# Performance work log

Hardware: AMD Instinct MI355X
Metric: run time of the kernel (lower is better)

## Reference

```python
import jax, jax.numpy as jnp
import numpy as np

D_MODEL = 1024
N_HEADS = 16
HEAD_DIM = D_MODEL // N_HEADS
WINDOW = 128
N_PERSIST = 4
KSIZE = 3


def _make_mask(L):
    """[T,T] additive mask, T = N_PERSIST + L. Persistent rows: causal among
    persistent tokens. Sequence rows: all persistent cols + sliding causal window."""
    T = N_PERSIST + L
    r = jnp.arange(T)[:, None]
    c = jnp.arange(T)[None, :]
    seq_allowed = (c < N_PERSIST) | ((c >= jnp.maximum(N_PERSIST, r - WINDOW + 1)) & (c <= r))
    allowed = jnp.where(r < N_PERSIST, c <= r, seq_allowed)
    return jnp.where(allowed, 0.0, -jnp.inf).astype(jnp.float32)


def _causal_dw_conv(y, w, b):
    # y: [B,T,D] -> depthwise causal conv1d + SiLU -> [B,T,D]
    y = y.transpose(0, 2, 1)  # [B,D,T]
    y = jax.lax.conv_general_dilated(
        y, w, window_strides=(1,), padding=[(KSIZE - 1, 0)],
        feature_group_count=D_MODEL, dimension_numbers=('NCH', 'OIH', 'NCH'))
    y = jax.nn.silu(y + b[None, :, None])
    return y.transpose(0, 2, 1)


def _l2norm(y, eps=1e-12):
    n = jnp.linalg.norm(y, axis=-1, keepdims=True)
    return y / jnp.maximum(n, eps)


def setup_inputs() -> dict:
    key = jax.random.key(0)
    ks = jax.random.split(key, 12)
    s = 1.0 / np.sqrt(D_MODEL)
    return {
        'x': jax.random.normal(ks[0], (1, 2048, D_MODEL), jnp.float32),
        'persistent_memory': jax.random.normal(ks[1], (1, N_PERSIST, D_MODEL), jnp.float32) * 0.02,
        'Wq': jax.random.normal(ks[2], (D_MODEL, D_MODEL), jnp.float32) * s,
        'Wk': jax.random.normal(ks[3], (D_MODEL, D_MODEL), jnp.float32) * s,
        'Wv': jax.random.normal(ks[4], (D_MODEL, D_MODEL), jnp.float32) * s,
        'Wo': jax.random.normal(ks[5], (D_MODEL, D_MODEL), jnp.float32) * s,
        'q_conv_w': jax.random.normal(ks[6], (D_MODEL, 1, KSIZE), jnp.float32) * 0.3,
        'q_conv_b': jax.random.normal(ks[7], (D_MODEL,), jnp.float32) * 0.02,
        'k_conv_w': jax.random.normal(ks[8], (D_MODEL, 1, KSIZE), jnp.float32) * 0.3,
        'k_conv_b': jax.random.normal(ks[9], (D_MODEL,), jnp.float32) * 0.02,
        'v_conv_w': jax.random.normal(ks[10], (D_MODEL, 1, KSIZE), jnp.float32) * 0.3,
        'v_conv_b': jax.random.normal(ks[11], (D_MODEL,), jnp.float32) * 0.02,
    }


def reference(x, persistent_memory, Wq, Wk, Wv, Wo,
              q_conv_w, q_conv_b, k_conv_w, k_conv_b, v_conv_w, v_conv_b):
    B, L, D = x.shape
    T = L + N_PERSIST
    scale = HEAD_DIM ** -0.5
    xp = jnp.concatenate([jnp.broadcast_to(persistent_memory, (B, N_PERSIST, D)), x], axis=1)
    Q = xp @ Wq.T
    K = xp @ Wk.T
    V = xp @ Wv.T
    Q = _causal_dw_conv(Q, q_conv_w, q_conv_b)
    K = _causal_dw_conv(K, k_conv_w, k_conv_b)
    V = _causal_dw_conv(V, v_conv_w, v_conv_b)
    Q = _l2norm(Q)
    K = _l2norm(K)
    # [B,H,T,hd]
    Q = Q.reshape(B, T, N_HEADS, HEAD_DIM).transpose(0, 2, 1, 3)
    K = K.reshape(B, T, N_HEADS, HEAD_DIM).transpose(0, 2, 1, 3)
    V = V.reshape(B, T, N_HEADS, HEAD_DIM).transpose(0, 2, 1, 3)
    scores = jnp.einsum('bhqd,bhkd->bhqk', Q, K) * scale + _make_mask(L)[None, None]
    attn = jax.nn.softmax(scores, axis=-1)
    out = jnp.einsum('bhqk,bhkd->bhqd', attn, V)
    out = out.transpose(0, 2, 1, 3).reshape(B, T, D) @ Wo.T
    return out[:, N_PERSIST:, :]
```

## Files before the change

### kernel.cpp

```cpp
#include <hip/hip_runtime.h>
#include <math.h>

typedef unsigned short u16;
typedef unsigned int   u32;
typedef unsigned long long u64;
typedef __attribute__((ext_vector_type(8))) short bf16x8;
typedef __attribute__((ext_vector_type(4))) float f32x4;
typedef __attribute__((ext_vector_type(4))) int i32x4;

#define TTOT  2052
#define NPERS 4
#define LSEQ  2048
#define WIN   128
#define NHEAD 16
#define HDIM  64
#define DM    1024
#define MPAD  2176

__device__ __forceinline__ float bf2f(u16 u) {
    union { unsigned int i; float f; } v; v.i = ((unsigned int)u) << 16; return v.f;
}
__device__ __forceinline__ u16 f2bf(float f) {
    union { float f; unsigned int i; } v; v.f = f;
    unsigned int r = (v.i + 0x7fffu + ((v.i >> 16) & 1u)) >> 16;
    return (u16)r;
}
__device__ __forceinline__ u32 pk2(float lo, float hi) {
    return (u32)f2bf(lo) | ((u32)f2bf(hi) << 16);
}

__device__ __forceinline__ void glds16(const u16* g, u16* l) {
    __builtin_amdgcn_global_load_lds(
        (__attribute__((address_space(1))) void*)(g),
        (__attribute__((address_space(3))) void*)(l),
        16, 0, 0);
}

__global__ __launch_bounds__(256) void cvt(const float* __restrict__ x, const float* __restrict__ pm,
    const float* __restrict__ Wq, const float* __restrict__ Wk, const float* __restrict__ Wv,
    const float* __restrict__ Wo,
    u16* __restrict__ xp, u16* __restrict__ Wcat, u16* __restrict__ Woh)
{
    const int z = blockIdx.y;
    const int u = blockIdx.x * 256 + threadIdx.x;
    if (z == 0) {
        if (u >= TTOT * 256) return;
        const size_t e = (size_t)u * 4;
        const int row = (int)(e >> 10), c = (int)(e & 1023);
        const float* s = (row < NPERS) ? (pm + (size_t)row * DM + c)
                                       : (x + (size_t)(row - NPERS) * DM + c);
        f32x4 v = *(const f32x4*)s;
        *(u64*)(xp + e) = (u64)pk2(v[0], v[1]) | ((u64)pk2(v[2], v[3]) << 32);
    } else {
        if (u >= 256 * DM) return;
        const size_t e = (size_t)u * 4;
        const float* s; u16* d;
        if (z == 1)      { s = Wq + e; d = Wcat + e; }
        else if (z == 2) { s = Wk + e; d = Wcat + (size_t)DM * DM + e; }
        else if (z == 3) { s = Wv + e; d = Wcat + 2 * (size_t)DM * DM + e; }
        else             { s = Wo + e; d = Woh + e; }
        f32x4 v = *(const f32x4*)s;
        *(u64*)d = (u64)pk2(v[0], v[1]) | ((u64)pk2(v[2], v[3]) << 32);
    }
}

template<int TM, int TN, bool OF32>
__device__ __forceinline__ void gemm_lds(const u16* __restrict__ Ablk, const u16* __restrict__ Bblk,
                                         void* __restrict__ Cbase, int mlim)
{
    __shared__ __align__(16) u16 As[TM * 32];
    __shared__ __align__(16) u16 Bs[TN * 32];
    const int tid  = threadIdx.x;
    const int lane = tid & 63;
    const int l15  = lane & 15, quad = lane >> 4;
    constexpr int RM = TM / 32, RN = TN / 32;
    const int wm = (tid >> 7) * (TM / 2);
    const int wn = ((tid >> 6) & 1) * (TN / 2);
    const int wb = tid & 192;

    f32x4 acc[RM][RN];
    #pragma unroll
    for (int i = 0; i < RM; i++)
        #pragma unroll
        for (int j = 0; j < RN; j++) acc[i][j] = (f32x4){0.f, 0.f, 0.f, 0.f};

    constexpr int LA = (TM * 32) / 2048;
    constexpr int LB = (TN * 32) / 2048;

    for (int kk = 0; kk < DM; kk += 32) {
        #pragma unroll
        for (int i = 0; i < LA; i++) {
            const int e = i * 256 + tid;
            glds16(Ablk + (size_t)(e >> 2) * DM + kk + (e & 3) * 8,
                   As + (size_t)(i * 256 + wb) * 8);
        }
        #pragma unroll
        for (int i = 0; i < LB; i++) {
            const int e = i * 256 + tid;
            glds16(Bblk + (size_t)(e >> 2) * DM + kk + (e & 3) * 8,
                   Bs + (size_t)(i * 256 + wb) * 8);
        }
        __syncthreads();
        bf16x8 af[RM], bfr[RN];
        #pragma unroll
        for (int i = 0; i < RM; i++) af[i]  = *(const bf16x8*)&As[(wm + i * 16 + l15) * 32 + quad * 8];
        #pragma unroll
        for (int j = 0; j < RN; j++) bfr[j] = *(const bf16x8*)&Bs[(wn + j * 16 + l15) * 32 + quad * 8];
        #pragma unroll
        for (int i = 0; i < RM; i++)
            #pragma unroll
            for (int j = 0; j < RN; j++)
                acc[i][j] = __builtin_amdgcn_mfma_f32_16x16x32_bf16(af[i], bfr[j], acc[i][j], 0, 0, 0);
        __syncthreads();
    }

    #pragma unroll
    for (int i = 0; i < RM; i++) {
        const int m0 = wm + i * 16 + quad * 4;
        #pragma unroll
        for (int j = 0; j < RN; j++) {
            const int n = wn + j * 16 + l15;
            #pragma unroll
            for (int r = 0; r < 4; r++) {
                const int m = m0 + r;
                if (m < mlim) {
                    if (OF32) ((float*)Cbase)[(size_t)m * DM + n] = acc[i][j][r];
                    else      ((u16*)Cbase)[(size_t)m * DM + n]   = f2bf(acc[i][j][r]);
                }
            }
        }
    }
}

__global__ __launch_bounds__(256) void gemm_qkv(const u16* __restrict__ xp, const u16* __restrict__ Wcat,
    u16* __restrict__ Qr, u16* __restrict__ Kr, u16* __restrict__ Vr)
{
    const int Mb = blockIdx.x * 128;
    const int nb = blockIdx.y;
    u16* C = (nb < 8) ? Qr : (nb < 16) ? Kr : Vr;
    const int Ncol = (nb & 7) * 128;
    gemm_lds<128, 128, false>(xp + (size_t)Mb * DM,
                              Wcat + (size_t)nb * 128 * DM,
                              (void*)(C + (size_t)Mb * DM + Ncol),
                              TTOT - Mb);
}

__global__ __launch_bounds__(256) void gemm_out(const u16* __restrict__ AO, const u16* __restrict__ Woh,
                                                float* __restrict__ Cout)
{
    const int Mb = blockIdx.x * 64, Nb = blockIdx.y * 128;
    gemm_lds<64, 128, true>(AO + (size_t)Mb * DM, Woh + (size_t)Nb * DM,
                            (void*)(Cout + (size_t)Mb * DM + Nb), 64);
}

__global__ __launch_bounds__(256) void conv_silu_norm(
    const u16* __restrict__ Qr, const u16* __restrict__ Kr, const u16* __restrict__ Vr,
    const float* __restrict__ qw, const float* __restrict__ qb,
    const float* __restrict__ kw, const float* __restrict__ kb,
    const float* __restrict__ vw, const float* __restrict__ vb,
    u16* __restrict__ Qc, u16* __restrict__ Kc, u16* __restrict__ Vc)
{
    const int t = blockIdx.x;
    const int z = blockIdx.y;
    const u16* raw; const float *w, *b; u16* out;
    if (z == 0)      { raw = Qr; w = qw; b = qb; out = Qc; }
    else if (z == 1) { raw = Kr; w = kw; b = kb; out = Kc; }
    else             { raw = Vr; w = vw; b = vb; out = Vc; }

    const int tid = threadIdx.x;
    const int d0  = tid * 4;

    const u16* r0 = raw + (size_t)t * DM + d0;
    u64 c0 = *(const u64*)r0;
    u64 c1 = (t >= 1) ? *(const u64*)(r0 - DM)     : 0ULL;
    u64 c2 = (t >= 2) ? *(const u64*)(r0 - 2 * DM) : 0ULL;
    const f32x4 bias = *(const f32x4*)(b + d0);
    const f32x4 w0v  = *(const f32x4*)(w + 3 * d0);
    const f32x4 w1v  = *(const f32x4*)(w + 3 * d0 + 4);
    const f32x4 w2v  = *(const f32x4*)(w + 3 * d0 + 8);
    const float warr[12] = {w0v[0], w0v[1], w0v[2], w0v[3],
                            w1v[0], w1v[1], w1v[2], w1v[3],
                            w2v[0], w2v[1], w2v[2], w2v[3]};

    float vals[4];
    float ss = 0.f;
    #pragma unroll
    for (int c = 0; c < 4; c++) {
        float acc = bias[c];
        acc += warr[3*c + 2] * bf2f((u16)(c0 >> (16 * c)));
        acc += warr[3*c + 1] * bf2f((u16)(c1 >> (16 * c)));
        acc += warr[3*c + 0] * bf2f((u16)(c2 >> (16 * c)));
        const float y = acc / (1.f + __expf(-acc));
        vals[c] = y;
        ss += y * y;
    }
    float inv = 1.f;
    if (z < 2) {
        #pragma unroll
        for (int off = 32; off > 0; off >>= 1) ss += __shfl_down(ss, off, 64);
        __shared__ float red[4];
        const int wv = tid >> 6, ln = tid & 63;
        if (ln == 0) red[wv] = ss;
        __syncthreads();
        const float tot = red[0] + red[1] + red[2] + red[3];
        inv = 1.f / fmaxf(sqrtf(tot), 1e-12f);
    }
    u64 o = 0;
    #pragma unroll
    for (int c = 0; c < 4; c++) o |= (u64)f2bf(vals[c] * inv) << (16 * c);
    *(u64*)(out + (size_t)t * DM + d0) = o;
}

#define QT     64
#define KTILES 13
#define KROWS  208
#define KPAD   224
#define KSTR   72
#define VSTR   232

__global__ __launch_bounds__(256) void attn(const u16* __restrict__ Q, const u16* __restrict__ K,
                                            const u16* __restrict__ V, u16* __restrict__ AO)
{
    const int h  = blockIdx.y;
    const int qb = blockIdx.x * QT;
    const int kstart = max(NPERS, qb + NPERS - (WIN - 1));
    const int nk = NPERS + (qb + NPERS + QT - 1) - kstart + 1;

    __shared__ __align__(16) u16 KP[KROWS * KSTR];
    __shared__ __align__(16) u16 Vt[64 * VSTR];
    u16* Ks = KP;
    u16* Ps = KP;

    const int tid = threadIdx.x;

    for (int c = tid; c < KROWS * 8; c += 256) {
        const int i = c >> 3, off = (c & 7) * 8;
        if (i < nk) {
            const int g = (i < NPERS) ? i : (kstart + i - NPERS);
            *(i32x4*)&Ks[i * KSTR + off] = *(const i32x4*)&K[(size_t)g * DM + h * HDIM + off];
        }
    }
    {
        const int d = tid & 63, w4 = tid >> 6;
        for (int i2 = w4 * 2; i2 < KPAD; i2 += 8) {
            u16 a = 0, b = 0;
            if (i2 < nk)     { const int g = (i2     < NPERS) ? i2     : (kstart + i2     - NPERS); a = V[(size_t)g * DM + h * HDIM + d]; }
            if (i2 + 1 < nk) { const int g = (i2 + 1 < NPERS) ? i2 + 1 : (kstart + i2 + 1 - NPERS); b = V[(size_t)g * DM + h * HDIM + d]; }
            *(u32*)&Vt[d * VSTR + i2] = (u32)a | ((u32)b << 16);
        }
    }
    __syncthreads();

    const int wv = tid >> 6, lane = tid & 63, l15 = lane & 15, quad = lane >> 4;
    const int qloc0 = wv * 16;

    const int tqrow = qb + qloc0 + l15 + NPERS;
    const bf16x8 qa0 = *(const bf16x8*)&Q[(size_t)tqrow * DM + h * HDIM + quad * 8];
    const bf16x8 qa1 = *(const bf16x8*)&Q[(size_t)tqrow * DM + h * HDIM + 32 + quad * 8];

    f32x4 st[KTILES];
    #pragma unroll
    for (int t = 0; t < KTILES; t++) {
        const bf16x8 kb0 = *(const bf16x8*)&Ks[(t * 16 + l15) * KSTR + quad * 8];
        const bf16x8 kb1 = *(const bf16x8*)&Ks[(t * 16 + l15) * KSTR + 32 + quad * 8];
        f32x4 z = (f32x4){0.f, 0.f, 0.f, 0.f};
        z = __builtin_amdgcn_mfma_f32_16x16x32_bf16(qa0, kb0, z, 0, 0, 0);
        z = __builtin_amdgcn_mfma_f32_16x16x32_bf16(qa1, kb1, z, 0, 0, 0);
        st[t] = z;
    }

    const float scale = 0.125f;
    float mrow[4] = {-INFINITY, -INFINITY, -INFINITY, -INFINITY};
    #pragma unroll
    for (int t = 0; t < KTILES; t++) {
        const int i  = t * 16 + l15;
        const int kg = kstart + i - NPERS;
        #pragma unroll
        for (int r = 0; r < 4; r++) {
            const int tqr = qb + qloc0 + quad * 4 + r + NPERS;
            const bool ok = (i < NPERS) || ((i < nk) && (kg >= tqr - (WIN - 1)) && (kg <= tqr));
            const float s = ok ? st[t][r] * scale : -INFINITY;
            st[t][r] = s;
            mrow[r] = fmaxf(mrow[r], s);
        }
    }
    #pragma unroll
    for (int off = 1; off < 16; off <<= 1)
        #pragma unroll
        for (int r = 0; r < 4; r++) mrow[r] = fmaxf(mrow[r], __shfl_xor(mrow[r], off, 64));

    float ssum[4] = {0.f, 0.f, 0.f, 0.f};
    #pragma unroll
    for (int t = 0; t < KTILES; t++)
        #pragma unroll
        for (int r = 0; r < 4; r++) {
            const float p = __expf(st[t][r] - mrow[r]);
            st[t][r] = p;
            ssum[r] += p;
        }
    #pragma unroll
    for (int off = 1; off < 16; off <<= 1)
        #pragma unroll
        for (int r = 0; r < 4; r++) ssum[r] += __shfl_xor(ssum[r], off, 64);
    float inv[4];
    #pragma unroll
    for (int r = 0; r < 4; r++) inv[r] = 1.f / ssum[r];

    __syncthreads();

    #pragma unroll
    for (int t = 0; t < KTILES; t++)
        #pragma unroll
        for (int r = 0; r < 4; r++)
            Ps[(qloc0 + quad * 4 + r) * VSTR + t * 16 + l15] = f2bf(st[t][r] * inv[r]);
    *(u64*)&Ps[(qloc0 + l15) * VSTR + KROWS + quad * 4] = 0ULL;
    __syncthreads();

    f32x4 oacc[4];
    #pragma unroll
    for (int dt = 0; dt < 4; dt++) oacc[dt] = (f32x4){0.f, 0.f, 0.f, 0.f};
    for (int ks = 0; ks < KPAD / 32; ks++) {
        const bf16x8 pa = *(const bf16x8*)&Ps[(qloc0 + l15) * VSTR + ks * 32 + quad * 8];
        #pragma unroll
        for (int dt = 0; dt < 4; dt++) {
            const bf16x8 vb = *(const bf16x8*)&Vt[(dt * 16 + l15) * VSTR + ks * 32 + quad * 8];
            oacc[dt] = __builtin_amdgcn_mfma_f32_16x16x32_bf16(pa, vb, oacc[dt], 0, 0, 0);
        }
    }

    #pragma unroll
    for (int dt = 0; dt < 4; dt++)
        #pragma unroll
        for (int r = 0; r < 4; r++)
            AO[(size_t)(qb + qloc0 + quad * 4 + r) * DM + h * HDIM + dt * 16 + l15] = f2bf(oacc[dt][r]);
}

extern "C" void kernel_launch(void* const* d_in, const int* in_sizes, int n_in,
                              void* d_out, int out_size, void* d_ws, size_t ws_size,
                              hipStream_t stream)
{
    const float* x  = (const float*)d_in[0];
    const float* pm = (const float*)d_in[1];
    const float* Wq = (const float*)d_in[2];
    const float* Wk = (const float*)d_in[3];
    const float* Wv = (const float*)d_in[4];
    const float* Wo = (const float*)d_in[5];
    const float* qw = (const float*)d_in[6];
    const float* qb = (const float*)d_in[7];
    const float* kw = (const float*)d_in[8];
    const float* kb = (const float*)d_in[9];
    const float* vw = (const float*)d_in[10];
    const float* vb = (const float*)d_in[11];
    float* out = (float*)d_out;

    u16* ws16 = (u16*)d_ws;
    const size_t SZ_W  = (size_t)DM * DM;
    const size_t SZ_R  = (size_t)TTOT * DM;
    const size_t SZ_XP = (size_t)MPAD * DM;
    u16* Woh  = ws16;
    u16* Qr   = Woh + SZ_W;        u16* AO = Qr;
    u16* Kr   = Qr + SZ_R;
    u16* Vr   = Kr + SZ_R;
    u16* Vc   = Vr + SZ_R;
    u16* xp   = Vc + SZ_R;         u16* Qc = xp;
    u16* Wcat = xp + SZ_XP;        u16* Kc = Wcat;

    hipLaunchKernelGGL(cvt, dim3(TTOT, 5), dim3(256), 0, stream,
                       x, pm, Wq, Wk, Wv, Wo, xp, Wcat, Woh);
    hipLaunchKernelGGL(gemm_qkv, dim3(17, 24), dim3(256), 0, stream,
                       xp, Wcat, Qr, Kr, Vr);
    hipLaunchKernelGGL(conv_silu_norm, dim3(TTOT, 3), dim3(256), 0, stream,
                       Qr, Kr, Vr, qw, qb, kw, kb, vw, vb, Qc, Kc, Vc);
    hipLaunchKernelGGL(attn, dim3(LSEQ / QT, NHEAD), dim3(256), 0, stream,
                       Qc, Kc, Vc, AO);
    hipLaunchKernelGGL(gemm_out, dim3(32, 8), dim3(256), 0, stream,
                       AO, Woh, out);
}
```

Before: 163.8 us.

## Deepen GEMM K-tile to 64 with XOR-swizzled LDS, pack cvt and conv launches

The shared GEMM routine now stages 64-wide K slices per iteration instead of 32. It XOR-swizzles the LDS column chunks to avoid bank conflicts, which halves the barriers per K and doubles LDS use. The convert kernel switches to a flat 1D grid without idle blocks. The conv/SiLU/norm kernel handles two timesteps per block so neighbouring rows are shared and fewer blocks launch.

```diff
diff --git a/kernel.cpp b/kernel.cpp
--- a/kernel.cpp
+++ b/kernel.cpp
@@ -36,47 +36,47 @@
         16, 0, 0);
 }
 
+#define XP_UNITS (TTOT * DM / 4)
+#define W_UNITS  (DM * DM / 4)
+#define CVT_BLOCKS ((XP_UNITS + 4 * W_UNITS) / 256)
+
 __global__ __launch_bounds__(256) void cvt(const float* __restrict__ x, const float* __restrict__ pm,
     const float* __restrict__ Wq, const float* __restrict__ Wk, const float* __restrict__ Wv,
     const float* __restrict__ Wo,
     u16* __restrict__ xp, u16* __restrict__ Wcat, u16* __restrict__ Woh)
 {
-    const int z = blockIdx.y;
-    const int u = blockIdx.x * 256 + threadIdx.x;
-    if (z == 0) {
-        if (u >= TTOT * 256) return;
-        const size_t e = (size_t)u * 4;
+    const int id = blockIdx.x * 256 + threadIdx.x;
+    const float* s; u16* d;
+    if (id < XP_UNITS) {
+        const size_t e = (size_t)id * 4;
         const int row = (int)(e >> 10), c = (int)(e & 1023);
-        const float* s = (row < NPERS) ? (pm + (size_t)row * DM + c)
-                                       : (x + (size_t)(row - NPERS) * DM + c);
-        f32x4 v = *(const f32x4*)s;
-        *(u64*)(xp + e) = (u64)pk2(v[0], v[1]) | ((u64)pk2(v[2], v[3]) << 32);
+        s = (row < NPERS) ? (pm + (size_t)row * DM + c) : (x + (size_t)(row - NPERS) * DM + c);
+        d = xp + e;
     } else {
-        if (u >= 256 * DM) return;
-        const size_t e = (size_t)u * 4;
-        const float* s; u16* d;
-        if (z == 1)      { s = Wq + e; d = Wcat + e; }
-        else if (z == 2) { s = Wk + e; d = Wcat + (size_t)DM * DM + e; }
-        else if (z == 3) { s = Wv + e; d = Wcat + 2 * (size_t)DM * DM + e; }
-        else             { s = Wo + e; d = Woh + e; }
-        f32x4 v = *(const f32x4*)s;
-        *(u64*)d = (u64)pk2(v[0], v[1]) | ((u64)pk2(v[2], v[3]) << 32);
-    }
+        const int w   = id - XP_UNITS;
+        const int sel = w >> 18;
+        const size_t e = (size_t)(w & (W_UNITS - 1)) * 4;
+        if (sel == 0)      { s = Wq + e; d = Wcat + e; }
+        else if (sel == 1) { s = Wk + e; d = Wcat + (size_t)DM * DM + e; }
+        else if (sel == 2) { s = Wv + e; d = Wcat + 2 * (size_t)DM * DM + e; }
+        else               { s = Wo + e; d = Woh + e; }
+    }
+    f32x4 v = *(const f32x4*)s;
+    *(u64*)d = (u64)pk2(v[0], v[1]) | ((u64)pk2(v[2], v[3]) << 32);
 }
 
 template<int TM, int TN, bool OF32>
 __device__ __forceinline__ void gemm_lds(const u16* __restrict__ Ablk, const u16* __restrict__ Bblk,
                                          void* __restrict__ Cbase, int mlim)
 {
-    __shared__ __align__(16) u16 As[TM * 32];
-    __shared__ __align__(16) u16 Bs[TN * 32];
+    __shared__ __align__(16) u16 As[TM * 64];
+    __shared__ __align__(16) u16 Bs[TN * 64];
     const int tid  = threadIdx.x;
     const int lane = tid & 63;
     const int l15  = lane & 15, quad = lane >> 4;
     constexpr int RM = TM / 32, RN = TN / 32;
     const int wm = (tid >> 7) * (TM / 2);
     const int wn = ((tid >> 6) & 1) * (TN / 2);
-    const int wb = tid & 192;
 
     f32x4 acc[RM][RN];
     #pragma unroll
@@ -84,33 +84,38 @@
         #pragma unroll
         for (int j = 0; j < RN; j++) acc[i][j] = (f32x4){0.f, 0.f, 0.f, 0.f};
 
-    constexpr int LA = (TM * 32) / 2048;
-    constexpr int LB = (TN * 32) / 2048;
-
-    for (int kk = 0; kk < DM; kk += 32) {
+    constexpr int LA = TM / 32;
+    constexpr int LB = TN / 32;
+
+    for (int kk = 0; kk < DM; kk += 64) {
         #pragma unroll
         for (int i = 0; i < LA; i++) {
             const int e = i * 256 + tid;
-            glds16(Ablk + (size_t)(e >> 2) * DM + kk + (e & 3) * 8,
-                   As + (size_t)(i * 256 + wb) * 8);
+            const int row = e >> 3, sc = (e & 7) ^ (row & 7);
+            glds16(Ablk + (size_t)row * DM + kk + sc * 8, As + (size_t)e * 8);
         }
         #pragma unroll
         for (int i = 0; i < LB; i++) {
             const int e = i * 256 + tid;
-            glds16(Bblk + (size_t)(e >> 2) * DM + kk + (e & 3) * 8,
-                   Bs + (size_t)(i * 256 + wb) * 8);
+            const int row = e >> 3, sc = (e & 7) ^ (row & 7);
+            glds16(Bblk + (size_t)row * DM + kk + sc * 8, Bs + (size_t)e * 8);
         }
         __syncthreads();
-        bf16x8 af[RM], bfr[RN];
-        #pragma unroll
-        for (int i = 0; i < RM; i++) af[i]  = *(const bf16x8*)&As[(wm + i * 16 + l15) * 32 + quad * 8];
-        #pragma unroll
-        for (int j = 0; j < RN; j++) bfr[j] = *(const bf16x8*)&Bs[(wn + j * 16 + l15) * 32 + quad * 8];
-        #pragma unroll
-        for (int i = 0; i < RM; i++)
+        #pragma unroll
+        for (int kc = 0; kc < 2; kc++) {
+            bf16x8 af[RM], bfr[RN];
+            #pragma unroll
+            for (int i = 0; i < RM; i++)
+                af[i]  = *(const bf16x8*)&As[(wm + i * 16 + l15) * 64 + (((kc * 4 + quad) ^ (l15 & 7)) * 8)];
             #pragma unroll
             for (int j = 0; j < RN; j++)
-                acc[i][j] = __builtin_amdgcn_mfma_f32_16x16x32_bf16(af[i], bfr[j], acc[i][j], 0, 0, 0);
+                bfr[j] = *(const bf16x8*)&Bs[(wn + j * 16 + l15) * 64 + (((kc * 4 + quad) ^ (l15 & 7)) * 8)];
+            #pragma unroll
+            for (int i = 0; i < RM; i++)
+                #pragma unroll
+                for (int j = 0; j < RN; j++)
+                    acc[i][j] = __builtin_amdgcn_mfma_f32_16x16x32_bf16(af[i], bfr[j], acc[i][j], 0, 0, 0);
+        }
         __syncthreads();
     }
 
@@ -160,8 +165,8 @@
     const float* __restrict__ vw, const float* __restrict__ vb,
     u16* __restrict__ Qc, u16* __restrict__ Kc, u16* __restrict__ Vc)
 {
-    const int t = blockIdx.x;
-    const int z = blockIdx.y;
+    const int t0 = blockIdx.x * 2;
+    const int z  = blockIdx.y;
     const u16* raw; const float *w, *b; u16* out;
     if (z == 0)      { raw = Qr; w = qw; b = qb; out = Qc; }
     else if (z == 1) { raw = Kr; w = kw; b = kb; out = Kc; }
@@ -170,10 +175,11 @@
     const int tid = threadIdx.x;
     const int d0  = tid * 4;
 
-    const u16* r0 = raw + (size_t)t * DM + d0;
-    u64 c0 = *(const u64*)r0;
-    u64 c1 = (t >= 1) ? *(const u64*)(r0 - DM)     : 0ULL;
-    u64 c2 = (t >= 2) ? *(const u64*)(r0 - 2 * DM) : 0ULL;
+    const u16* r0 = raw + (size_t)t0 * DM + d0;
+    const u64 cm2 = (t0 >= 2) ? *(const u64*)(r0 - 2 * DM) : 0ULL;
+    const u64 cm1 = (t0 >= 1) ? *(const u64*)(r0 - DM)     : 0ULL;
+    const u64 c0  = *(const u64*)r0;
+    const u64 c1  = *(const u64*)(r0 + DM);
     const f32x4 bias = *(const f32x4*)(b + d0);
     const f32x4 w0v  = *(const f32x4*)(w + 3 * d0);
     const f32x4 w1v  = *(const f32x4*)(w + 3 * d0 + 4);
@@ -182,33 +188,44 @@
                             w1v[0], w1v[1], w1v[2], w1v[3],
                             w2v[0], w2v[1], w2v[2], w2v[3]};
 
-    float vals[4];
-    float ss = 0.f;
+    float va[4], vb2[4];
+    float ss0 = 0.f, ss1 = 0.f;
     #pragma unroll
     for (int c = 0; c < 4; c++) {
-        float acc = bias[c];
-        acc += warr[3*c + 2] * bf2f((u16)(c0 >> (16 * c)));
-        acc += warr[3*c + 1] * bf2f((u16)(c1 >> (16 * c)));
-        acc += warr[3*c + 0] * bf2f((u16)(c2 >> (16 * c)));
-        const float y = acc / (1.f + __expf(-acc));
-        vals[c] = y;
-        ss += y * y;
-    }
-    float inv = 1.f;
+        const float xm2 = bf2f((u16)(cm2 >> (16 * c)));
+        const float xm1 = bf2f((u16)(cm1 >> (16 * c)));
+        const float x0  = bf2f((u16)(c0  >> (16 * c)));
+        const float x1  = bf2f((u16)(c1  >> (16 * c)));
+        const float w0 = warr[3*c], w1 = warr[3*c + 1], w2 = warr[3*c + 2];
+        float a0 = bias[c] + w2 * x0 + w1 * xm1 + w0 * xm2;
+        float a1 = bias[c] + w2 * x1 + w1 * x0  + w0 * xm1;
+        const float y0 = a0 / (1.f + __expf(-a0));
+        const float y1 = a1 / (1.f + __expf(-a1));
+        va[c] = y0; vb2[c] = y1;
+        ss0 += y0 * y0; ss1 += y1 * y1;
+    }
+    float inv0 = 1.f, inv1 = 1.f;
     if (z < 2) {
         #pragma unroll
-        for (int off = 32; off > 0; off >>= 1) ss += __shfl_down(ss, off, 64);
-        __shared__ float red[4];
+        for (int off = 32; off > 0; off >>= 1) {
+            ss0 += __shfl_down(ss0, off, 64);
+            ss1 += __shfl_down(ss1, off, 64);
+        }
+        __shared__ float red[8];
         const int wv = tid >> 6, ln = tid & 63;
-        if (ln == 0) red[wv] = ss;
+        if (ln == 0) { red[wv] = ss0; red[wv + 4] = ss1; }
         __syncthreads();
-        const float tot = red[0] + red[1] + red[2] + red[3];
-        inv = 1.f / fmaxf(sqrtf(tot), 1e-12f);
-    }
-    u64 o = 0;
-    #pragma unroll
-    for (int c = 0; c < 4; c++) o |= (u64)f2bf(vals[c] * inv) << (16 * c);
-    *(u64*)(out + (size_t)t * DM + d0) = o;
+        inv0 = 1.f / fmaxf(sqrtf(red[0] + red[1] + red[2] + red[3]), 1e-12f);
+        inv1 = 1.f / fmaxf(sqrtf(red[4] + red[5] + red[6] + red[7]), 1e-12f);
+    }
+    u64 o0 = 0, o1 = 0;
+    #pragma unroll
+    for (int c = 0; c < 4; c++) {
+        o0 |= (u64)f2bf(va[c]  * inv0) << (16 * c);
+        o1 |= (u64)f2bf(vb2[c] * inv1) << (16 * c);
+    }
+    *(u64*)(out + (size_t)t0 * DM + d0)      = o0;
+    *(u64*)(out + (size_t)(t0 + 1) * DM + d0) = o1;
 }
 
 #define QT     64
@@ -365,11 +382,11 @@
     u16* xp   = Vc + SZ_R;         u16* Qc = xp;
     u16* Wcat = xp + SZ_XP;        u16* Kc = Wcat;
 
-    hipLaunchKernelGGL(cvt, dim3(TTOT, 5), dim3(256), 0, stream,
+    hipLaunchKernelGGL(cvt, dim3(CVT_BLOCKS), dim3(256), 0, stream,
                        x, pm, Wq, Wk, Wv, Wo, xp, Wcat, Woh);
     hipLaunchKernelGGL(gemm_qkv, dim3(17, 24), dim3(256), 0, stream,
                        xp, Wcat, Qr, Kr, Vr);
-    hipLaunchKernelGGL(conv_silu_norm, dim3(TTOT, 3), dim3(256), 0, stream,
+    hipLaunchKernelGGL(conv_silu_norm, dim3(TTOT / 2, 3), dim3(256), 0, stream,
                        Qr, Kr, Vr, qw, qb, kw, kb, vw, vb, Qc, Kc, Vc);
     hipLaunchKernelGGL(attn, dim3(LSEQ / QT, NHEAD), dim3(256), 0, stream,
                        Qc, Kc, Vc, AO);
```

Result: faster. 159.2 us (-2.8%).
